# Kernel optimization log

Hardware: AMD Instinct MI355X
Metric: run time of the kernel (lower is better)

## Reference

```python
import jax, jax.numpy as jnp
import numpy as np

VOCAB = 50257
DIM = 768
RANK = 16
ALPHA = 32.0
SCALING = ALPHA / RANK


def setup_inputs() -> dict:
    key = jax.random.key(0)
    k1, k2, k3, k4 = jax.random.split(key, 4)
    inputs = jax.random.randint(k1, (8, 2048), 0, VOCAB, dtype=jnp.int32)
    embeddings = jax.random.uniform(k2, (VOCAB, DIM), dtype=jnp.float32, minval=-0.05, maxval=0.05)
    # he_uniform for lora_a: limit = sqrt(6 / fan_in), fan_in = VOCAB
    limit = float(np.sqrt(6.0 / VOCAB))
    lora_a = jax.random.uniform(k3, (VOCAB, RANK), dtype=jnp.float32, minval=-limit, maxval=limit)
    # lora_b initialized zeros per module, but use small random so grads are nontrivial
    lora_b = jax.random.normal(k4, (RANK, DIM), dtype=jnp.float32) * 0.01
    magnitude = jnp.ones((DIM,), dtype=jnp.float32)
    return {"inputs": inputs, "embeddings": embeddings, "lora_a": lora_a,
            "lora_b": lora_b, "magnitude": magnitude}


def reference(inputs, embeddings, lora_a, lora_b, magnitude):
    # W = m * (W0 + scaling * A @ B) / ||W0 + scaling * A @ B||_col
    combined = embeddings + jnp.matmul(lora_a, lora_b) * SCALING  # [V, D]
    col_norms = jnp.sqrt(jnp.sum(jnp.square(combined), axis=0, keepdims=True))  # [1, D]
    col_norms = jnp.maximum(col_norms, 1e-8)
    dora_table = combined / col_norms * magnitude[None, :]  # [V, D]
    return jnp.take(dora_table, inputs, axis=0)  # [B, S, D]
```

## Files before the change

### kernel.cpp

```cpp
#include <hip/hip_runtime.h>
#include <math.h>

#define VOCAB 50257
#define DIM 768
#define RANK 16
#define SCALING 2.0f

constexpr int P1_BLOCKS = 2048;
constexpr int P1_THREADS = 192;
constexpr int ROWS_PER_BLOCK = (VOCAB + P1_BLOCKS - 1) / P1_BLOCKS;
constexpr int RED_THREADS = 256;
constexpr int TOKENS_PER_BLOCK = 8;
constexpr int G_THREADS = 192;

__global__ __launch_bounds__(P1_THREADS) void dora_pass1(
    const float* __restrict__ emb, const float* __restrict__ lora_a,
    const float* __restrict__ lora_b, float* __restrict__ partials) {
  const int t = threadIdx.x;
  const int c4 = t * 4;

  float4 B[RANK];
#pragma unroll
  for (int k = 0; k < RANK; ++k)
    B[k] = *reinterpret_cast<const float4*>(lora_b + k * DIM + c4);

  const int r0 = blockIdx.x * ROWS_PER_BLOCK;
  const int r1 = min(r0 + ROWS_PER_BLOCK, VOCAB);

  float4 acc = make_float4(0.f, 0.f, 0.f, 0.f);
  for (int v = r0; v < r1; ++v) {
    const float* __restrict__ arow = lora_a + (size_t)v * RANK;
    const float4 e = *reinterpret_cast<const float4*>(emb + (size_t)v * DIM + c4);
    float dx = 0.f, dy = 0.f, dz = 0.f, dw = 0.f;
#pragma unroll
    for (int k = 0; k < RANK; ++k) {
      const float a = arow[k];
      dx = fmaf(a, B[k].x, dx);
      dy = fmaf(a, B[k].y, dy);
      dz = fmaf(a, B[k].z, dz);
      dw = fmaf(a, B[k].w, dw);
    }
    const float cx = fmaf(SCALING, dx, e.x);
    const float cy = fmaf(SCALING, dy, e.y);
    const float cz = fmaf(SCALING, dz, e.z);
    const float cw = fmaf(SCALING, dw, e.w);
    acc.x = fmaf(cx, cx, acc.x);
    acc.y = fmaf(cy, cy, acc.y);
    acc.z = fmaf(cz, cz, acc.z);
    acc.w = fmaf(cw, cw, acc.w);
  }
  *reinterpret_cast<float4*>(partials + (size_t)blockIdx.x * DIM + c4) = acc;
}

__global__ __launch_bounds__(RED_THREADS) void dora_reduce(
    const float* __restrict__ partials, const float* __restrict__ magnitude,
    float* __restrict__ scale) {
  const int c = blockIdx.x;
  const int t = threadIdx.x;
  float s = 0.f;
#pragma unroll
  for (int k = 0; k < P1_BLOCKS / RED_THREADS; ++k)
    s += partials[(size_t)(t + k * RED_THREADS) * DIM + c];

#pragma unroll
  for (int off = 32; off > 0; off >>= 1) s += __shfl_down(s, off);

  __shared__ float lds[RED_THREADS / 64];
  if ((t & 63) == 0) lds[t >> 6] = s;
  __syncthreads();
  if (t == 0) {
    float tot = 0.f;
#pragma unroll
    for (int w = 0; w < RED_THREADS / 64; ++w) tot += lds[w];
    const float norm = fmaxf(sqrtf(tot), 1e-8f);
    scale[c] = magnitude[c] / norm;
  }
}

__global__ __launch_bounds__(G_THREADS) void dora_gather(
    const int* __restrict__ tokens, const float* __restrict__ emb,
    const float* __restrict__ lora_a, const float* __restrict__ lora_b,
    const float* __restrict__ scale, float* __restrict__ out, int n_tokens) {
  const int t = threadIdx.x;
  const int c4 = t * 4;

  float4 B[RANK];
#pragma unroll
  for (int k = 0; k < RANK; ++k)
    B[k] = *reinterpret_cast<const float4*>(lora_b + k * DIM + c4);
  const float4 sc = *reinterpret_cast<const float4*>(scale + c4);

  const int tok0 = blockIdx.x * TOKENS_PER_BLOCK;
#pragma unroll
  for (int i = 0; i < TOKENS_PER_BLOCK; ++i) {
    const int tok = tok0 + i;
    if (tok >= n_tokens) break;
    const int id = tokens[tok];
    const float* __restrict__ arow = lora_a + (size_t)id * RANK;
    const float4 e = *reinterpret_cast<const float4*>(emb + (size_t)id * DIM + c4);
    float dx = 0.f, dy = 0.f, dz = 0.f, dw = 0.f;
#pragma unroll
    for (int k = 0; k < RANK; ++k) {
      const float a = arow[k];
      dx = fmaf(a, B[k].x, dx);
      dy = fmaf(a, B[k].y, dy);
      dz = fmaf(a, B[k].z, dz);
      dw = fmaf(a, B[k].w, dw);
    }
    float4 o;
    o.x = fmaf(SCALING, dx, e.x) * sc.x;
    o.y = fmaf(SCALING, dy, e.y) * sc.y;
    o.z = fmaf(SCALING, dz, e.z) * sc.z;
    o.w = fmaf(SCALING, dw, e.w) * sc.w;
    *reinterpret_cast<float4*>(out + (size_t)tok * DIM + c4) = o;
  }
}

extern "C" void kernel_launch(void* const* d_in, const int* in_sizes, int n_in,
                              void* d_out, int out_size, void* d_ws, size_t ws_size,
                              hipStream_t stream) {
  const int*   tokens    = (const int*)d_in[0];
  const float* emb       = (const float*)d_in[1];
  const float* lora_a    = (const float*)d_in[2];
  const float* lora_b    = (const float*)d_in[3];
  const float* magnitude = (const float*)d_in[4];
  float* out = (float*)d_out;

  const int n_tokens = in_sizes[0];

  float* partials = (float*)d_ws;
  float* scale    = (float*)d_ws + (size_t)P1_BLOCKS * DIM;

  dora_pass1<<<P1_BLOCKS, P1_THREADS, 0, stream>>>(emb, lora_a, lora_b, partials);
  dora_reduce<<<DIM, RED_THREADS, 0, stream>>>(partials, magnitude, scale);

  const int gather_blocks = (n_tokens + TOKENS_PER_BLOCK - 1) / TOKENS_PER_BLOCK;
  dora_gather<<<gather_blocks, G_THREADS, 0, stream>>>(tokens, emb, lora_a, lora_b,
                                                       scale, out, n_tokens);
}
```

Before: 272.1 us.

## Software-prefetch rows in pass1/gather and coalesce the column-norm reduction

Pass1 and gather now load the next row's embedding and lora_a values before computing the current row, so memory latency overlaps with the FMAs. Both kernels get occupancy hints in their launch bounds. The reduce kernel is restructured so that 12 blocks of 1024 threads each handle 64 columns with coalesced row reads, replacing 768 blocks that did strided single-column reads. Gather tokens per block drops from 8 to 4. The prefetch adds register pressure and one redundant load at the end of each row range.

```diff
diff --git a/kernel.cpp b/kernel.cpp
--- a/kernel.cpp
+++ b/kernel.cpp
@@ -9,11 +9,15 @@
 constexpr int P1_BLOCKS = 2048;
 constexpr int P1_THREADS = 192;
 constexpr int ROWS_PER_BLOCK = (VOCAB + P1_BLOCKS - 1) / P1_BLOCKS;
-constexpr int RED_THREADS = 256;
-constexpr int TOKENS_PER_BLOCK = 8;
+
+constexpr int RED_THREADS = 1024;
+constexpr int RED_WAVES = RED_THREADS / 64;
+constexpr int RED_BLOCKS = DIM / 64;
+
+constexpr int TOKENS_PER_BLOCK = 4;
 constexpr int G_THREADS = 192;
 
-__global__ __launch_bounds__(P1_THREADS) void dora_pass1(
+__global__ __launch_bounds__(P1_THREADS, 4) void dora_pass1(
     const float* __restrict__ emb, const float* __restrict__ lora_a,
     const float* __restrict__ lora_b, float* __restrict__ partials) {
   const int t = threadIdx.x;
@@ -26,28 +30,42 @@
 
   const int r0 = blockIdx.x * ROWS_PER_BLOCK;
   const int r1 = min(r0 + ROWS_PER_BLOCK, VOCAB);
+  float4 acc = make_float4(0.f, 0.f, 0.f, 0.f);
 
-  float4 acc = make_float4(0.f, 0.f, 0.f, 0.f);
-  for (int v = r0; v < r1; ++v) {
-    const float* __restrict__ arow = lora_a + (size_t)v * RANK;
-    const float4 e = *reinterpret_cast<const float4*>(emb + (size_t)v * DIM + c4);
-    float dx = 0.f, dy = 0.f, dz = 0.f, dw = 0.f;
+  if (r0 < r1) {
+    float4 e = *reinterpret_cast<const float4*>(emb + (size_t)r0 * DIM + c4);
+    float a[RANK];
 #pragma unroll
-    for (int k = 0; k < RANK; ++k) {
-      const float a = arow[k];
-      dx = fmaf(a, B[k].x, dx);
-      dy = fmaf(a, B[k].y, dy);
-      dz = fmaf(a, B[k].z, dz);
-      dw = fmaf(a, B[k].w, dw);
+    for (int k = 0; k < RANK; ++k) a[k] = lora_a[(size_t)r0 * RANK + k];
+
+    for (int v = r0; v < r1; ++v) {
+      const int vp = min(v + 1, r1 - 1);
+      const float4 e_next = *reinterpret_cast<const float4*>(emb + (size_t)vp * DIM + c4);
+      float a_next[RANK];
+#pragma unroll
+      for (int k = 0; k < RANK; ++k) a_next[k] = lora_a[(size_t)vp * RANK + k];
+
+      float dx = 0.f, dy = 0.f, dz = 0.f, dw = 0.f;
+#pragma unroll
+      for (int k = 0; k < RANK; ++k) {
+        dx = fmaf(a[k], B[k].x, dx);
+        dy = fmaf(a[k], B[k].y, dy);
+        dz = fmaf(a[k], B[k].z, dz);
+        dw = fmaf(a[k], B[k].w, dw);
+      }
+      const float cx = fmaf(SCALING, dx, e.x);
+      const float cy = fmaf(SCALING, dy, e.y);
+      const float cz = fmaf(SCALING, dz, e.z);
+      const float cw = fmaf(SCALING, dw, e.w);
+      acc.x = fmaf(cx, cx, acc.x);
+      acc.y = fmaf(cy, cy, acc.y);
+      acc.z = fmaf(cz, cz, acc.z);
+      acc.w = fmaf(cw, cw, acc.w);
+
+      e = e_next;
+#pragma unroll
+      for (int k = 0; k < RANK; ++k) a[k] = a_next[k];
     }
-    const float cx = fmaf(SCALING, dx, e.x);
-    const float cy = fmaf(SCALING, dy, e.y);
-    const float cz = fmaf(SCALING, dz, e.z);
-    const float cw = fmaf(SCALING, dw, e.w);
-    acc.x = fmaf(cx, cx, acc.x);
-    acc.y = fmaf(cy, cy, acc.y);
-    acc.z = fmaf(cz, cz, acc.z);
-    acc.w = fmaf(cw, cw, acc.w);
   }
   *reinterpret_cast<float4*>(partials + (size_t)blockIdx.x * DIM + c4) = acc;
 }
@@ -55,29 +73,28 @@
 __global__ __launch_bounds__(RED_THREADS) void dora_reduce(
     const float* __restrict__ partials, const float* __restrict__ magnitude,
     float* __restrict__ scale) {
-  const int c = blockIdx.x;
-  const int t = threadIdx.x;
+  const int lane = threadIdx.x & 63;
+  const int w = threadIdx.x >> 6;
+  const int c = blockIdx.x * 64 + lane;
+
   float s = 0.f;
-#pragma unroll
-  for (int k = 0; k < P1_BLOCKS / RED_THREADS; ++k)
-    s += partials[(size_t)(t + k * RED_THREADS) * DIM + c];
+#pragma unroll 8
+  for (int r = w; r < P1_BLOCKS; r += RED_WAVES)
+    s += partials[(size_t)r * DIM + c];
 
-#pragma unroll
-  for (int off = 32; off > 0; off >>= 1) s += __shfl_down(s, off);
-
-  __shared__ float lds[RED_THREADS / 64];
-  if ((t & 63) == 0) lds[t >> 6] = s;
+  __shared__ float lds[RED_WAVES][64];
+  lds[w][lane] = s;
   __syncthreads();
-  if (t == 0) {
+  if (w == 0) {
     float tot = 0.f;
 #pragma unroll
-    for (int w = 0; w < RED_THREADS / 64; ++w) tot += lds[w];
+    for (int i = 0; i < RED_WAVES; ++i) tot += lds[i][lane];
     const float norm = fmaxf(sqrtf(tot), 1e-8f);
     scale[c] = magnitude[c] / norm;
   }
 }
 
-__global__ __launch_bounds__(G_THREADS) void dora_gather(
+__global__ __launch_bounds__(G_THREADS, 4) void dora_gather(
     const int* __restrict__ tokens, const float* __restrict__ emb,
     const float* __restrict__ lora_a, const float* __restrict__ lora_b,
     const float* __restrict__ scale, float* __restrict__ out, int n_tokens) {
@@ -91,28 +108,45 @@
   const float4 sc = *reinterpret_cast<const float4*>(scale + c4);
 
   const int tok0 = blockIdx.x * TOKENS_PER_BLOCK;
+  int id[TOKENS_PER_BLOCK];
+#pragma unroll
+  for (int i = 0; i < TOKENS_PER_BLOCK; ++i)
+    id[i] = tokens[min(tok0 + i, n_tokens - 1)];
+
+  float4 e = *reinterpret_cast<const float4*>(emb + (size_t)id[0] * DIM + c4);
+  float a[RANK];
+#pragma unroll
+  for (int k = 0; k < RANK; ++k) a[k] = lora_a[(size_t)id[0] * RANK + k];
+
 #pragma unroll
   for (int i = 0; i < TOKENS_PER_BLOCK; ++i) {
-    const int tok = tok0 + i;
-    if (tok >= n_tokens) break;
-    const int id = tokens[tok];
-    const float* __restrict__ arow = lora_a + (size_t)id * RANK;
-    const float4 e = *reinterpret_cast<const float4*>(emb + (size_t)id * DIM + c4);
+    const int ip = min(i + 1, TOKENS_PER_BLOCK - 1);
+    const float4 e_next = *reinterpret_cast<const float4*>(emb + (size_t)id[ip] * DIM + c4);
+    float a_next[RANK];
+#pragma unroll
+    for (int k = 0; k < RANK; ++k) a_next[k] = lora_a[(size_t)id[ip] * RANK + k];
+
     float dx = 0.f, dy = 0.f, dz = 0.f, dw = 0.f;
 #pragma unroll
     for (int k = 0; k < RANK; ++k) {
-      const float a = arow[k];
-      dx = fmaf(a, B[k].x, dx);
-      dy = fmaf(a, B[k].y, dy);
-      dz = fmaf(a, B[k].z, dz);
-      dw = fmaf(a, B[k].w, dw);
+      dx = fmaf(a[k], B[k].x, dx);
+      dy = fmaf(a[k], B[k].y, dy);
+      dz = fmaf(a[k], B[k].z, dz);
+      dw = fmaf(a[k], B[k].w, dw);
     }
     float4 o;
     o.x = fmaf(SCALING, dx, e.x) * sc.x;
     o.y = fmaf(SCALING, dy, e.y) * sc.y;
     o.z = fmaf(SCALING, dz, e.z) * sc.z;
     o.w = fmaf(SCALING, dw, e.w) * sc.w;
-    *reinterpret_cast<float4*>(out + (size_t)tok * DIM + c4) = o;
+
+    const int tok = tok0 + i;
+    if (tok < n_tokens)
+      *reinterpret_cast<float4*>(out + (size_t)tok * DIM + c4) = o;
+
+    e = e_next;
+#pragma unroll
+    for (int k = 0; k < RANK; ++k) a[k] = a_next[k];
   }
 }
 
@@ -132,7 +166,7 @@
   float* scale    = (float*)d_ws + (size_t)P1_BLOCKS * DIM;
 
   dora_pass1<<<P1_BLOCKS, P1_THREADS, 0, stream>>>(emb, lora_a, lora_b, partials);
-  dora_reduce<<<DIM, RED_THREADS, 0, stream>>>(partials, magnitude, scale);
+  dora_reduce<<<RED_BLOCKS, RED_THREADS, 0, stream>>>(partials, magnitude, scale);
 
   const int gather_blocks = (n_tokens + TOKENS_PER_BLOCK - 1) / TOKENS_PER_BLOCK;
   dora_gather<<<gather_blocks, G_THREADS, 0, stream>>>(tokens, emb, lora_a, lora_b,
```

Result: slower. 278.2 us (+2.2%).

## Fuse column-norm reduction into pass1 via atomics and last-block finalize

Applied to the files above, without the earlier changes.

Removes the separate reduce kernel and the per-block partials buffer. Each pass1 block atomically adds its column sums of squares into a global buffer, and the last block to finish, found with an atomic counter, computes the scale vector. It also halves the number of pass1 blocks so each processes more rows, and adds a small memset per call. The cost is atomic contention (1024 blocks × 768 float atomics) and run-to-run variation in float summation order.

```diff
diff --git a/kernel.cpp b/kernel.cpp
--- a/kernel.cpp
+++ b/kernel.cpp
@@ -6,16 +6,22 @@
 #define RANK 16
 #define SCALING 2.0f
 
-constexpr int P1_BLOCKS = 2048;
+constexpr int P1_BLOCKS = 1024;
 constexpr int P1_THREADS = 192;
-constexpr int ROWS_PER_BLOCK = (VOCAB + P1_BLOCKS - 1) / P1_BLOCKS;
-constexpr int RED_THREADS = 256;
-constexpr int TOKENS_PER_BLOCK = 8;
+constexpr int ROWS_PB = (VOCAB + P1_BLOCKS - 1) / P1_BLOCKS;
+
+constexpr int TOK_PB = 8;
 constexpr int G_THREADS = 192;
+
+constexpr size_t WS_SUMSQ_OFF = 0;
+constexpr size_t WS_COUNTER_OFF = 3072;
+constexpr size_t WS_SCALE_OFF = 3088;
 
 __global__ __launch_bounds__(P1_THREADS) void dora_pass1(
     const float* __restrict__ emb, const float* __restrict__ lora_a,
-    const float* __restrict__ lora_b, float* __restrict__ partials) {
+    const float* __restrict__ lora_b, const float* __restrict__ magnitude,
+    float* __restrict__ sumsq, float* __restrict__ scale,
+    unsigned* __restrict__ counter) {
   const int t = threadIdx.x;
   const int c4 = t * 4;
 
@@ -24,17 +30,16 @@
   for (int k = 0; k < RANK; ++k)
     B[k] = *reinterpret_cast<const float4*>(lora_b + k * DIM + c4);
 
-  const int r0 = blockIdx.x * ROWS_PER_BLOCK;
-  const int r1 = min(r0 + ROWS_PER_BLOCK, VOCAB);
-
+  const int r0 = blockIdx.x * ROWS_PB;
+  const int r1 = min(r0 + ROWS_PB, VOCAB);
   float4 acc = make_float4(0.f, 0.f, 0.f, 0.f);
+#pragma unroll 2
   for (int v = r0; v < r1; ++v) {
-    const float* __restrict__ arow = lora_a + (size_t)v * RANK;
     const float4 e = *reinterpret_cast<const float4*>(emb + (size_t)v * DIM + c4);
     float dx = 0.f, dy = 0.f, dz = 0.f, dw = 0.f;
 #pragma unroll
     for (int k = 0; k < RANK; ++k) {
-      const float a = arow[k];
+      const float a = lora_a[(size_t)v * RANK + k];
       dx = fmaf(a, B[k].x, dx);
       dy = fmaf(a, B[k].y, dy);
       dz = fmaf(a, B[k].z, dz);
@@ -49,31 +54,27 @@
     acc.z = fmaf(cz, cz, acc.z);
     acc.w = fmaf(cw, cw, acc.w);
   }
-  *reinterpret_cast<float4*>(partials + (size_t)blockIdx.x * DIM + c4) = acc;
-}
+  atomicAdd(&sumsq[c4 + 0], acc.x);
+  atomicAdd(&sumsq[c4 + 1], acc.y);
+  atomicAdd(&sumsq[c4 + 2], acc.z);
+  atomicAdd(&sumsq[c4 + 3], acc.w);
 
-__global__ __launch_bounds__(RED_THREADS) void dora_reduce(
-    const float* __restrict__ partials, const float* __restrict__ magnitude,
-    float* __restrict__ scale) {
-  const int c = blockIdx.x;
-  const int t = threadIdx.x;
-  float s = 0.f;
-#pragma unroll
-  for (int k = 0; k < P1_BLOCKS / RED_THREADS; ++k)
-    s += partials[(size_t)(t + k * RED_THREADS) * DIM + c];
-
-#pragma unroll
-  for (int off = 32; off > 0; off >>= 1) s += __shfl_down(s, off);
-
-  __shared__ float lds[RED_THREADS / 64];
-  if ((t & 63) == 0) lds[t >> 6] = s;
+  __threadfence();
   __syncthreads();
-  if (t == 0) {
-    float tot = 0.f;
-#pragma unroll
-    for (int w = 0; w < RED_THREADS / 64; ++w) tot += lds[w];
-    const float norm = fmaxf(sqrtf(tot), 1e-8f);
-    scale[c] = magnitude[c] / norm;
+  __shared__ unsigned is_last;
+  if (t == 0) is_last = (atomicAdd(counter, 1u) == P1_BLOCKS - 1) ? 1u : 0u;
+  __syncthreads();
+  if (is_last) {
+    const float sx = atomicAdd(&sumsq[c4 + 0], 0.0f);
+    const float sy = atomicAdd(&sumsq[c4 + 1], 0.0f);
+    const float sz = atomicAdd(&sumsq[c4 + 2], 0.0f);
+    const float sw = atomicAdd(&sumsq[c4 + 3], 0.0f);
+    float4 sc;
+    sc.x = magnitude[c4 + 0] / fmaxf(sqrtf(sx), 1e-8f);
+    sc.y = magnitude[c4 + 1] / fmaxf(sqrtf(sy), 1e-8f);
+    sc.z = magnitude[c4 + 2] / fmaxf(sqrtf(sz), 1e-8f);
+    sc.w = magnitude[c4 + 3] / fmaxf(sqrtf(sw), 1e-8f);
+    *reinterpret_cast<float4*>(scale + c4) = sc;
   }
 }
 
@@ -90,9 +91,9 @@
     B[k] = *reinterpret_cast<const float4*>(lora_b + k * DIM + c4);
   const float4 sc = *reinterpret_cast<const float4*>(scale + c4);
 
-  const int tok0 = blockIdx.x * TOKENS_PER_BLOCK;
+  const int tok0 = blockIdx.x * TOK_PB;
 #pragma unroll
-  for (int i = 0; i < TOKENS_PER_BLOCK; ++i) {
+  for (int i = 0; i < TOK_PB; ++i) {
     const int tok = tok0 + i;
     if (tok >= n_tokens) break;
     const int id = tokens[tok];
@@ -128,13 +129,17 @@
 
   const int n_tokens = in_sizes[0];
 
-  float* partials = (float*)d_ws;
-  float* scale    = (float*)d_ws + (size_t)P1_BLOCKS * DIM;
+  char* ws = (char*)d_ws;
+  float*    sumsq   = (float*)(ws + WS_SUMSQ_OFF);
+  unsigned* counter = (unsigned*)(ws + WS_COUNTER_OFF);
+  float*    scale   = (float*)(ws + WS_SCALE_OFF);
 
-  dora_pass1<<<P1_BLOCKS, P1_THREADS, 0, stream>>>(emb, lora_a, lora_b, partials);
-  dora_reduce<<<DIM, RED_THREADS, 0, stream>>>(partials, magnitude, scale);
+  hipMemsetAsync(ws, 0, WS_COUNTER_OFF + 4, stream);
 
-  const int gather_blocks = (n_tokens + TOKENS_PER_BLOCK - 1) / TOKENS_PER_BLOCK;
+  dora_pass1<<<P1_BLOCKS, P1_THREADS, 0, stream>>>(emb, lora_a, lora_b, magnitude,
+                                                   sumsq, scale, counter);
+
+  const int gather_blocks = (n_tokens + TOK_PB - 1) / TOK_PB;
   dora_gather<<<gather_blocks, G_THREADS, 0, stream>>>(tokens, emb, lora_a, lora_b,
                                                        scale, out, n_tokens);
 }
```

Result: slower. 383.0 us (+40.7%).
